# Kernel optimization log

Measured on AMD Instinct MI355X. Metric: run time of the kernel, lower is better.

Reference implementation:

```python
import jax, jax.numpy as jnp
import numpy as np

HID = 1024; INTER = 2048; NSTATE = 16; KCONV = 4; DTRANK = 64
NHEADS = 16; NKV = 4; HDIM = 64; VHDIM = 128; EPS = 1e-6
ATTN_H = HID; K_H = NKV * HDIM; V_H = NKV * VHDIM
LATENT = INTER + ATTN_H + K_H + V_H  # 3840


def rmsnorm(x, w, eps=EPS):
    return x * jax.lax.rsqrt(jnp.mean(x * x, axis=-1, keepdims=True) + eps) * w


def setup_inputs():
    key = jax.random.key(0)
    ks = jax.random.split(key, 8)
    B, S = 2, 2048
    s = 0.02
    x = jax.random.normal(ks[0], (B, S, HID), jnp.float32)
    W_in = jax.random.normal(ks[1], (LATENT + INTER, HID), jnp.float32) * s
    conv_w = jax.random.normal(ks[2], (INTER, KCONV), jnp.float32) * 0.2
    conv_b = jnp.zeros((INTER,), jnp.float32)
    W_x = jax.random.normal(ks[3], (DTRANK + 2 * NSTATE, INTER), jnp.float32) * s
    dt_ln_w = jnp.ones((DTRANK,), jnp.float32)
    B_ln_w = jnp.ones((NSTATE,), jnp.float32)
    C_ln_w = jnp.ones((NSTATE,), jnp.float32)
    W_dt = jax.random.normal(ks[4], (INTER, DTRANK), jnp.float32) * s
    b_dt = jnp.log(jnp.expm1(jnp.full((INTER,), 0.01, jnp.float32)))
    A_log = jnp.log(jnp.broadcast_to(jnp.arange(1, NSTATE + 1, dtype=jnp.float32)[None, :], (INTER, NSTATE)))
    D_param = jnp.ones((INTER,), jnp.float32)
    ln1_w = jnp.ones((INTER,), jnp.float32)
    ln2_w = jnp.ones((INTER,), jnp.float32)
    W_out = jax.random.normal(ks[5], (HID, INTER), jnp.float32) * s
    return {"x": x, "W_in": W_in, "conv_w": conv_w, "conv_b": conv_b, "W_x": W_x,
            "dt_ln_w": dt_ln_w, "B_ln_w": B_ln_w, "C_ln_w": C_ln_w, "W_dt": W_dt,
            "b_dt": b_dt, "A_log": A_log, "D_param": D_param, "ln1_w": ln1_w,
            "ln2_w": ln2_w, "W_out": W_out}


def reference(x, W_in, conv_w, conv_b, W_x, dt_ln_w, B_ln_w, C_ln_w, W_dt, b_dt,
              A_log, D_param, ln1_w, ln2_w, W_out):
    Bsz, S, _ = x.shape
    proj = x @ W_in.T  # [B,S,LATENT+INTER]
    q = proj[..., :ATTN_H]
    k = proj[..., ATTN_H:ATTN_H + K_H]
    v = proj[..., ATTN_H + K_H:ATTN_H + K_H + V_H]
    xs = proj[..., ATTN_H + K_H + V_H:LATENT]
    gate = proj[..., LATENT:]

    # depthwise causal conv1d + silu (causal_conv1d_fn)
    xt = xs.transpose(0, 2, 1)  # [B,D,S]
    xc = jax.lax.conv_general_dilated(xt, conv_w[:, None, :], (1,), [(KCONV - 1, 0)],
                                      feature_group_count=INTER,
                                      dimension_numbers=("NCH", "OIH", "NCH"))
    xc = jax.nn.silu(xc + conv_b[None, :, None]).transpose(0, 2, 1)  # [B,S,D]

    # input-dependent dt, B, C with inner RMSNorms
    ssm_p = xc @ W_x.T  # [B,S,DTRANK+2N]
    dt = rmsnorm(ssm_p[..., :DTRANK], dt_ln_w)
    Bm = rmsnorm(ssm_p[..., DTRANK:DTRANK + NSTATE], B_ln_w)
    Cm = rmsnorm(ssm_p[..., DTRANK + NSTATE:], C_ln_w)
    delta = jax.nn.softplus(dt @ W_dt.T + b_dt)  # [B,S,D] (delta_bias + softplus)
    A = -jnp.exp(A_log)  # [D,N]

    def step(h, inp):
        d_t, b_t, c_t, x_t = inp  # [B,D],[B,N],[B,N],[B,D]
        dA = jnp.exp(d_t[:, :, None] * A)  # [B,D,N]
        h = h * dA + (d_t * x_t)[:, :, None] * b_t[:, None, :]
        y = jnp.einsum("bdn,bn->bd", h, c_t)
        return h, y

    h0 = jnp.zeros((Bsz, INTER, NSTATE), x.dtype)
    _, ys = jax.lax.scan(step, h0, (delta.transpose(1, 0, 2), Bm.transpose(1, 0, 2),
                                    Cm.transpose(1, 0, 2), xc.transpose(1, 0, 2)))
    y = ys.transpose(1, 0, 2) + xc * D_param
    y = y * jax.nn.silu(gate)  # gated scan output [B,S,INTER]

    # causal GQA attention branch (no output proj; v_head_dim = INTER/NHEADS)
    qh = q.reshape(Bsz, S, NHEADS, HDIM).transpose(0, 2, 1, 3)
    kh = jnp.repeat(k.reshape(Bsz, S, NKV, HDIM), NHEADS // NKV, axis=2).transpose(0, 2, 1, 3)
    vh = jnp.repeat(v.reshape(Bsz, S, NKV, VHDIM), NHEADS // NKV, axis=2).transpose(0, 2, 1, 3)
    scores = jnp.einsum("bhqd,bhkd->bhqk", qh, kh) * (1.0 / float(np.sqrt(HDIM)))
    mask = jnp.tril(jnp.ones((S, S), bool))
    scores = jnp.where(mask, scores, jnp.finfo(scores.dtype).min)
    attn = jnp.einsum("bhqk,bhkd->bhqd", jax.nn.softmax(scores, axis=-1), vh)
    attn = attn.transpose(0, 2, 1, 3).reshape(Bsz, S, INTER)

    out = (rmsnorm(attn, ln1_w) + rmsnorm(y, ln2_w)) * 0.5
    return out @ W_out.T
```

## Files before the change

### kernel.cpp

```cpp
#include <hip/hip_runtime.h>
#include <stdint.h>

#define HID    1024
#define INTER  2048
#define NSTATE 16
#define DTRANK 64
#define NHEADS 16
#define NKV    4
#define HDIM   64
#define VHDIM  128
#define ATTN_H 1024
#define K_H    256
#define V_H    512
#define LATENT 3840
#define NCOLS  5888
#define BATCH  2
#define SEQ    2048
#define T_TOT  4096
#define NCHUNK 64
#define CHLEN  32
#define LOG2E  1.44269504f

typedef __bf16 bf16x8 __attribute__((ext_vector_type(8)));
typedef float  f32x4  __attribute__((ext_vector_type(4)));
typedef float  f32x4v __attribute__((ext_vector_type(4)));
typedef unsigned short u16x8 __attribute__((ext_vector_type(8)));

__device__ __forceinline__ float bf2f(unsigned short u) {
    return __uint_as_float(((unsigned int)u) << 16);
}
__device__ __forceinline__ unsigned short f2bf(float f) {
    unsigned int u = __float_as_uint(f);
    u = (u + 0x7fffu + ((u >> 16) & 1u)) >> 16;
    return (unsigned short)u;
}
__device__ __forceinline__ bf16x8 ldb8(const unsigned short* p) {
    return __builtin_bit_cast(bf16x8, *(const u16x8*)p);
}

typedef const __attribute__((address_space(1))) unsigned int* gas_ptr;
typedef __attribute__((address_space(3))) unsigned int* las_ptr;
__device__ __forceinline__ void load_lds16(const void* g, void* l) {
    __builtin_amdgcn_global_load_lds((gas_ptr)g, (las_ptr)l, 16, 0, 0);
}

__global__ void k_prep(const float* __restrict__ x, const float* __restrict__ W_in,
                       const float* __restrict__ W_dt, const float* __restrict__ W_out,
                       const float* __restrict__ W_x,
                       unsigned short* __restrict__ xbf, unsigned short* __restrict__ Winbf,
                       unsigned short* __restrict__ Wdtbf, unsigned short* __restrict__ Woutbf,
                       unsigned short* __restrict__ Wxpad) {
    int i = blockIdx.x * 256 + threadIdx.x;
    const float* src; unsigned short* dst; int off;
    if (i < 524288)        { src = x;     dst = xbf;    off = i; }
    else if (i < 1277952)  { src = W_in;  dst = Winbf;  off = i - 524288; }
    else if (i < 1294336)  { src = W_dt;  dst = Wdtbf;  off = i - 1277952; }
    else if (i < 1556480)  { src = W_out; dst = Woutbf; off = i - 1294336; }
    else {
        int e = (i - 1556480) * 8;
        int row = e >> 11, col = e & 2047;
        u16x8 o;
        if (row < DTRANK + 2 * NSTATE) {
#pragma unroll
            for (int k = 0; k < 8; k++) o[k] = f2bf(W_x[(size_t)row * INTER + col + k]);
        } else {
#pragma unroll
            for (int k = 0; k < 8; k++) o[k] = 0;
        }
        *(u16x8*)(Wxpad + e) = o;
        return;
    }
    f32x4v a = ((const f32x4v*)src)[2 * off];
    f32x4v b = ((const f32x4v*)src)[2 * off + 1];
    u16x8 o;
#pragma unroll
    for (int k = 0; k < 4; k++) { o[k] = f2bf(a[k]); o[k + 4] = f2bf(b[k]); }
    *(u16x8*)(dst + (size_t)off * 8) = o;
}

template <int OUT_MODE>
__launch_bounds__(256)
__global__ void k_gemm(const unsigned short* __restrict__ A, const unsigned short* __restrict__ B,
                       void* __restrict__ Cout, const float* __restrict__ bias,
                       int M, int N, int K, int lda, int ldb, int ldc) {
    __shared__ __align__(16) unsigned short As[128 * 64];
    __shared__ __align__(16) unsigned short Bs[128 * 64];
    const int tid = threadIdx.x;
    const int lane = tid & 63;
    const int w = tid >> 6;
    const int wm = w >> 1, wn = w & 1;
    const int nwg = gridDim.x * gridDim.y;
    int lin = blockIdx.y * gridDim.x + blockIdx.x;
    lin = (lin & 7) * (nwg >> 3) + (lin >> 3);
    const int bm = (lin / gridDim.x) * 128, bn = (lin % gridDim.x) * 128;
    const size_t koff = (OUT_MODE == 3) ? (size_t)blockIdx.z * K : 0;

    f32x4 acc[4][4];
#pragma unroll
    for (int i = 0; i < 4; i++)
#pragma unroll
        for (int j = 0; j < 4; j++) acc[i][j] = (f32x4){0.f, 0.f, 0.f, 0.f};

    const int nk = K >> 6;
    for (int ks = 0; ks < nk; ++ks) {
        const int k0 = ks << 6;
#pragma unroll
        for (int i = 0; i < 4; ++i) {
            int qb = (w << 6) + (i << 8);
            int q = qb + lane;
            int row = q >> 3, c = q & 7;
            int csrc = c ^ (row & 7);
            load_lds16(A + (size_t)(bm + row) * lda + koff + k0 + csrc * 8, As + qb * 8);
            load_lds16(B + (size_t)(bn + row) * ldb + koff + k0 + csrc * 8, Bs + qb * 8);
        }
        __syncthreads();
#pragma unroll
        for (int kk = 0; kk < 2; ++kk) {
            bf16x8 af[4], bfr[4];
#pragma unroll
            for (int mi = 0; mi < 4; mi++) {
                int row = (wm << 6) + (mi << 4) + (lane & 15);
                int c = (kk << 2) + (lane >> 4);
                af[mi] = ldb8(As + row * 64 + (c ^ (row & 7)) * 8);
            }
#pragma unroll
            for (int ni = 0; ni < 4; ni++) {
                int row = (wn << 6) + (ni << 4) + (lane & 15);
                int c = (kk << 2) + (lane >> 4);
                bfr[ni] = ldb8(Bs + row * 64 + (c ^ (row & 7)) * 8);
            }
#pragma unroll
            for (int mi = 0; mi < 4; mi++)
#pragma unroll
                for (int ni = 0; ni < 4; ni++)
                    acc[mi][ni] = __builtin_amdgcn_mfma_f32_16x16x32_bf16(af[mi], bfr[ni], acc[mi][ni], 0, 0, 0);
        }
        __syncthreads();
    }
#pragma unroll
    for (int mi = 0; mi < 4; mi++)
#pragma unroll
        for (int ni = 0; ni < 4; ni++)
#pragma unroll
            for (int r = 0; r < 4; r++) {
                int grow = bm + (wm << 6) + (mi << 4) + ((lane >> 4) << 2) + r;
                int gcol = bn + (wn << 6) + (ni << 4) + (lane & 15);
                float v = acc[mi][ni][r];
                if (OUT_MODE == 0) {
                    ((unsigned short*)Cout)[(size_t)grow * ldc + gcol] = f2bf(v);
                } else if (OUT_MODE == 1) {
                    ((float*)Cout)[(size_t)grow * ldc + gcol] = v;
                } else if (OUT_MODE == 3) {
                    ((float*)Cout)[(size_t)blockIdx.z * M * ldc + (size_t)grow * ldc + gcol] = v;
                } else {
                    v += bias[gcol];
                    v = (v > 20.f) ? v : log1pf(__expf(v));
                    ((unsigned short*)Cout)[(size_t)grow * ldc + gcol] = f2bf(v);
                }
            }
}

__global__ void k_conv(const unsigned short* __restrict__ proj, const float* __restrict__ conv_w,
                       const float* __restrict__ conv_b, unsigned short* __restrict__ xc) {
    int r = blockIdx.x;
    int d8 = threadIdx.x * 8;
    int t = r & (SEQ - 1);
    float accv[8];
#pragma unroll
    for (int i = 0; i < 8; i++) accv[i] = conv_b[d8 + i];
#pragma unroll
    for (int j = 0; j < 4; j++) {
        int tp = t - 3 + j;
        if (tp < 0) continue;
        u16x8 xv = *(const u16x8*)(proj + (size_t)(r - 3 + j) * NCOLS + (LATENT - INTER) + d8);
#pragma unroll
        for (int i = 0; i < 8; i++) accv[i] += conv_w[(d8 + i) * 4 + j] * bf2f(xv[i]);
    }
    u16x8 o;
#pragma unroll
    for (int i = 0; i < 8; i++) {
        float v = accv[i];
        v = v / (1.f + __expf(-v));
        o[i] = f2bf(v);
    }
    *(u16x8*)(xc + (size_t)r * INTER + d8) = o;
}

__global__ void k_rms3(const float* __restrict__ ssmp, const float* __restrict__ dt_w,
                       const float* __restrict__ B_w, const float* __restrict__ C_w,
                       unsigned short* __restrict__ dtbf, float* __restrict__ Bm, float* __restrict__ Cm) {
    int r = blockIdx.x;
    int tid = threadIdx.x;
    int lane = tid & 63, w = tid >> 6;
    int c = tid;
    float v = 0.f;
    if (c < 96) {
#pragma unroll
        for (int s = 0; s < 8; s++) v += ssmp[(size_t)s * (T_TOT * 128) + (size_t)r * 128 + c];
    }
    float s = v * v;
    if (w == 0) {
#pragma unroll
        for (int d = 1; d < 64; d <<= 1) s += __shfl_xor(s, d);
        float rms = rsqrtf(s * (1.f / 64.f) + 1e-6f);
        dtbf[(size_t)r * 64 + lane] = f2bf(v * rms * dt_w[lane]);
    } else {
#pragma unroll
        for (int d = 1; d < 16; d <<= 1) s += __shfl_xor(s, d);
        float rms = rsqrtf(s * (1.f / 16.f) + 1e-6f);
        if (lane < 16) Bm[(size_t)r * 16 + lane] = v * rms * B_w[lane];
        else if (lane < 32) Cm[(size_t)r * 16 + (lane - 16)] = v * rms * C_w[lane - 16];
    }
}

template <int PASS>
__launch_bounds__(256)
__global__ void k_scan_chunk(const unsigned short* __restrict__ deltabf, const unsigned short* __restrict__ xcbf,
                             const float* __restrict__ Bm, const float* __restrict__ Cm,
                             const float* __restrict__ A_log,
                             float* __restrict__ hend, float* __restrict__ sumd,
                             const float* __restrict__ hinit, unsigned short* __restrict__ ybf) {
    __shared__ __align__(16) unsigned short dltS[CHLEN * 256];
    __shared__ __align__(16) unsigned short xvS[CHLEN * 256];
    __shared__ __align__(16) float BsT[CHLEN * 16];
    __shared__ __align__(16) float CsT[CHLEN * 16];
    const int d0 = blockIdx.x * 256;
    const int c = blockIdx.y;
    const int b = blockIdx.z;
    const int tid = threadIdx.x, lane = tid & 63, w = tid >> 6;
    const int t0 = c * CHLEN;
    const size_t rowbase = (size_t)(b * SEQ + t0);

    float An[16];
    {
        const f32x4* ap = (const f32x4*)(A_log + (size_t)(d0 + tid) * 16);
#pragma unroll
        for (int n4 = 0; n4 < 4; n4++) {
            f32x4 av = ap[n4];
#pragma unroll
            for (int j = 0; j < 4; j++) An[n4 * 4 + j] = -LOG2E * __expf(av[j]);
        }
    }

#pragma unroll
    for (int i = 0; i < 4; ++i) {
        int qb = (w << 6) + (i << 8);
        int q = qb + lane;
        int t = q >> 5, coff = q & 31;
        load_lds16(deltabf + (rowbase + t) * INTER + d0 + coff * 8, dltS + qb * 8);
        load_lds16(xcbf + (rowbase + t) * INTER + d0 + coff * 8, xvS + qb * 8);
    }
    if (tid < 128) {
        ((f32x4*)BsT)[tid] = ((const f32x4*)(Bm + rowbase * 16))[tid];
        if (PASS == 2) ((f32x4*)CsT)[tid] = ((const f32x4*)(Cm + rowbase * 16))[tid];
    }
    __syncthreads();

    const size_t sidx = ((size_t)(c * BATCH + b) * INTER + d0 + tid) * 16;
    float h[16];
    if (PASS == 2) {
        const f32x4* hp = (const f32x4*)(hinit + sidx);
#pragma unroll
        for (int n4 = 0; n4 < 4; n4++) {
            f32x4 hv = hp[n4];
#pragma unroll
            for (int j = 0; j < 4; j++) h[n4 * 4 + j] = hv[j];
        }
    } else {
#pragma unroll
        for (int n = 0; n < 16; n++) h[n] = 0.f;
    }
    float sd = 0.f;
    for (int t = 0; t < CHLEN; ++t) {
        float dlt = bf2f(dltS[t * 256 + tid]);
        float xv = bf2f(xvS[t * 256 + tid]);
        float dx = dlt * xv;
        if (PASS == 0) sd += dlt;
        float y = 0.f;
#pragma unroll
        for (int n4 = 0; n4 < 4; ++n4) {
            f32x4 Bt = ((f32x4*)BsT)[t * 4 + n4];
            f32x4 Ct;
            if (PASS == 2) Ct = ((f32x4*)CsT)[t * 4 + n4];
#pragma unroll
            for (int j = 0; j < 4; ++j) {
                int n = n4 * 4 + j;
                float a = exp2f(dlt * An[n]);
                h[n] = h[n] * a + dx * Bt[j];
                if (PASS == 2) y += h[n] * Ct[j];
            }
        }
        if (PASS == 2) ybf[(rowbase + t) * INTER + d0 + tid] = f2bf(y);
    }
    if (PASS == 0) {
        f32x4* hp = (f32x4*)(hend + sidx);
#pragma unroll
        for (int n4 = 0; n4 < 4; n4++) {
            f32x4 hv;
#pragma unroll
            for (int j = 0; j < 4; j++) hv[j] = h[n4 * 4 + j];
            hp[n4] = hv;
        }
        sumd[(size_t)(c * BATCH + b) * INTER + d0 + tid] = sd;
    }
}

__global__ void k_scan_prop(const float* __restrict__ A_log, const float* __restrict__ hend,
                            const float* __restrict__ sumd, float* __restrict__ hinit) {
    const int tid = blockIdx.x * 256 + threadIdx.x;
    const int n = tid & 15;
    const int d = (tid >> 4) & (INTER - 1);
    const float An = -LOG2E * __expf(A_log[(size_t)d * 16 + n]);
    const int bd = tid >> 4;
    float h = 0.f;
#pragma unroll 1
    for (int cb = 0; cb < NCHUNK / 4; ++cb) {
        float he[4], sdv[4];
#pragma unroll
        for (int j = 0; j < 4; j++) {
            int c = cb * 4 + j;
            he[j] = hend[(size_t)c * 65536 + tid];
            sdv[j] = sumd[(size_t)c * 4096 + bd];
        }
#pragma unroll
        for (int j = 0; j < 4; j++) {
            int c = cb * 4 + j;
            hinit[(size_t)c * 65536 + tid] = h;
            h = he[j] + exp2f(An * sdv[j]) * h;
        }
    }
}

__launch_bounds__(256)
__global__ void k_attn(const unsigned short* __restrict__ proj, unsigned short* __restrict__ attn) {
    __shared__ __align__(16) unsigned short Ks[64 * 64];
    __shared__ __align__(16) unsigned short Vt[128 * 64];
    __shared__ __align__(16) unsigned short Ps[4 * 16 * 64];
    const int pair = blockIdx.x;
    const int h = blockIdx.y;
    const int b = blockIdx.z;
    const int g = h >> 2;
    const int tid = threadIdx.x, lane = tid & 63, w = tid >> 6;
    const int l15 = lane & 15, hi = lane >> 4;

    const int krow = tid >> 3, kc = tid & 7;
    const int kp2 = (tid & 31) * 2, vb = tid >> 5;

    const unsigned short* kbase = proj + (size_t)(b * SEQ) * NCOLS + ATTN_H + g * HDIM;
    const unsigned short* vbase = proj + (size_t)(b * SEQ) * NCOLS + (ATTN_H + K_H) + g * VHDIM;

    u16x8 krA[2], vrA[2][2], krB[2], vrB[2][2];

    auto LOAD = [&](u16x8* kr, u16x8 (*vr)[2], int kv) {
        const unsigned short* kp_ = kbase + (size_t)(kv + krow) * NCOLS + kc * 8;
        kr[0] = *(const u16x8*)kp_;
        kr[1] = *(const u16x8*)(kp_ + (size_t)32 * NCOLS);
        const unsigned short* vp_ = vbase + (size_t)(kv + kp2) * NCOLS + vb * 8;
        vr[0][0] = *(const u16x8*)vp_;
        vr[0][1] = *(const u16x8*)(vp_ + NCOLS);
        vr[1][0] = *(const u16x8*)(vp_ + 64);
        vr[1][1] = *(const u16x8*)(vp_ + NCOLS + 64);
    };
    auto WRITE = [&](u16x8* kr, u16x8 (*vr)[2]) {
        int ksw = (kc ^ (krow & 7)) << 3;
        *(u16x8*)&Ks[krow * 64 + ksw] = kr[0];
        *(u16x8*)&Ks[(krow + 32) * 64 + ksw] = kr[1];
#pragma unroll
        for (int hf = 0; hf < 2; hf++) {
            u16x8 va = vr[hf][0], vb2 = vr[hf][1];
#pragma unroll
            for (int i = 0; i < 8; i++) {
                unsigned int pk = (unsigned int)va[i] | ((unsigned int)vb2[i] << 16);
                int r = (vb + hf * 8) * 8 + i;
                *(unsigned int*)&Vt[r * 64 + (((kp2 >> 3) ^ (r & 7)) << 3) + (kp2 & 7)] = pk;
            }
        }
    };

    const float SC = 0.18033688f;

    for (int phase = 0; phase < 2; ++phase) {
        const int qt = (phase == 0) ? (31 - pair) : pair;
        const int qw = qt * 64 + w * 16;
        const int ntiles = qt + 1;

        bf16x8 qf[2];
        {
            int qr = qw + l15;
            const unsigned short* qp = proj + (size_t)(b * SEQ + qr) * NCOLS + h * HDIM + hi * 8;
            qf[0] = ldb8(qp);
            qf[1] = ldb8(qp + 32);
        }
        f32x4 O[8];
#pragma unroll
        for (int vf = 0; vf < 8; vf++) O[vf] = (f32x4){0.f, 0.f, 0.f, 0.f};
        float l_[4] = {0.f, 0.f, 0.f, 0.f};

        auto COMPUTE = [&](int kv, bool MASK) {
            const int pbase = w * 1024;
            f32x4 sv[4];
#pragma unroll
            for (int cf = 0; cf < 4; ++cf) {
                f32x4 s = (f32x4){0.f, 0.f, 0.f, 0.f};
                int row = cf * 16 + l15;
#pragma unroll
                for (int kk = 0; kk < 2; ++kk) {
                    bf16x8 kb = ldb8(&Ks[row * 64 + ((((kk << 2) + hi) ^ (row & 7)) << 3)]);
                    s = __builtin_amdgcn_mfma_f32_16x16x32_bf16(qf[kk], kb, s, 0, 0, 0);
                }
                sv[cf] = s;
            }
            const int qi0 = qw + (hi << 2);
#pragma unroll
            for (int cf = 0; cf < 4; ++cf) {
                int ki = kv + cf * 16 + l15;
#pragma unroll
                for (int rg = 0; rg < 4; ++rg) {
                    float v;
                    if (MASK) v = (ki <= qi0 + rg) ? exp2f(sv[cf][rg] * SC) : 0.f;
                    else      v = exp2f(sv[cf][rg] * SC);
                    l_[rg] += v;
                    int pr = (hi << 2) + rg;
                    int pc = cf * 16 + l15;
                    Ps[pbase + pr * 64 + (((pc >> 3) ^ (pr & 7)) << 3) + (pc & 7)] = f2bf(v);
                }
            }
            bf16x8 pa0 = ldb8(&Ps[pbase + l15 * 64 + ((hi ^ (l15 & 7)) << 3)]);
            bf16x8 pa1 = ldb8(&Ps[pbase + l15 * 64 + (((4 + hi) ^ (l15 & 7)) << 3)]);
#pragma unroll
            for (int vf = 0; vf < 8; ++vf) {
                int vr_ = vf * 16 + l15;
                bf16x8 v0 = ldb8(&Vt[vr_ * 64 + ((hi ^ (vr_ & 7)) << 3)]);
                bf16x8 v1 = ldb8(&Vt[vr_ * 64 + (((4 + hi) ^ (vr_ & 7)) << 3)]);
                O[vf] = __builtin_amdgcn_mfma_f32_16x16x32_bf16(pa0, v0, O[vf], 0, 0, 0);
                O[vf] = __builtin_amdgcn_mfma_f32_16x16x32_bf16(pa1, v1, O[vf], 0, 0, 0);
            }
        };

        LOAD(krA, vrA, 0);
        bool useA = true;
        for (int j = 0; j < ntiles; ++j) {
            if (useA) {
                WRITE(krA, vrA);
                if (j + 1 < ntiles) LOAD(krB, vrB, (j + 1) * 64);
            } else {
                WRITE(krB, vrB);
                if (j + 1 < ntiles) LOAD(krA, vrA, (j + 1) * 64);
            }
            __syncthreads();
            COMPUTE(j * 64, j == ntiles - 1);
            __syncthreads();
            useA = !useA;
        }

#pragma unroll
        for (int dd = 1; dd < 16; dd <<= 1)
#pragma unroll
            for (int rg = 0; rg < 4; ++rg) l_[rg] += __shfl_xor(l_[rg], dd);
#pragma unroll
        for (int rg = 0; rg < 4; ++rg) {
            float inv = 1.f / l_[rg];
            int grow = b * SEQ + qw + (hi << 2) + rg;
#pragma unroll
            for (int vf = 0; vf < 8; ++vf) {
                int gcol = h * VHDIM + vf * 16 + l15;
                attn[(size_t)grow * INTER + gcol] = f2bf(O[vf][rg] * inv);
            }
        }
    }
}

__launch_bounds__(256)
__global__ void k_fuse(const unsigned short* __restrict__ attn, const unsigned short* __restrict__ ybf,
                       const unsigned short* __restrict__ xc, const unsigned short* __restrict__ proj,
                       const float* __restrict__ Dp, const float* __restrict__ ln1,
                       const float* __restrict__ ln2, unsigned short* __restrict__ fused) {
    __shared__ float red[8];
    int r = blockIdx.x, tid = threadIdx.x;
    int c8 = tid * 8;
    u16x8 av = *(const u16x8*)(attn + (size_t)r * INTER + c8);
    u16x8 yv8 = *(const u16x8*)(ybf + (size_t)r * INTER + c8);
    u16x8 xv8 = *(const u16x8*)(xc + (size_t)r * INTER + c8);
    u16x8 gv8 = *(const u16x8*)(proj + (size_t)r * NCOLS + LATENT + c8);
    float a_[8], y_[8];
    float ssa = 0.f, ssy = 0.f;
#pragma unroll
    for (int i = 0; i < 8; i++) {
        float a = bf2f(av[i]);
        float yv = bf2f(yv8[i]) + bf2f(xv8[i]) * Dp[c8 + i];
        float gg = bf2f(gv8[i]);
        yv *= gg / (1.f + __expf(-gg));
        a_[i] = a; y_[i] = yv;
        ssa += a * a; ssy += yv * yv;
    }
#pragma unroll
    for (int d = 1; d < 64; d <<= 1) { ssa += __shfl_xor(ssa, d); ssy += __shfl_xor(ssy, d); }
    int w = tid >> 6, lane = tid & 63;
    if (lane == 0) { red[w * 2] = ssa; red[w * 2 + 1] = ssy; }
    __syncthreads();
    ssa = red[0] + red[2] + red[4] + red[6];
    ssy = red[1] + red[3] + red[5] + red[7];
    float ra = rsqrtf(ssa * (1.f / 2048.f) + 1e-6f);
    float ry = rsqrtf(ssy * (1.f / 2048.f) + 1e-6f);
    u16x8 o;
#pragma unroll
    for (int i = 0; i < 8; i++) {
        float v = (a_[i] * ra * ln1[c8 + i] + y_[i] * ry * ln2[c8 + i]) * 0.5f;
        o[i] = f2bf(v);
    }
    *(u16x8*)(fused + (size_t)r * INTER + c8) = o;
}

extern "C" void kernel_launch(void* const* d_in, const int* in_sizes, int n_in,
                              void* d_out, int out_size, void* d_ws, size_t ws_size,
                              hipStream_t stream) {
    const float* x      = (const float*)d_in[0];
    const float* W_in   = (const float*)d_in[1];
    const float* conv_w = (const float*)d_in[2];
    const float* conv_b = (const float*)d_in[3];
    const float* W_x    = (const float*)d_in[4];
    const float* dt_w   = (const float*)d_in[5];
    const float* B_w    = (const float*)d_in[6];
    const float* C_w    = (const float*)d_in[7];
    const float* W_dt   = (const float*)d_in[8];
    const float* b_dt   = (const float*)d_in[9];
    const float* A_log  = (const float*)d_in[10];
    const float* Dp     = (const float*)d_in[11];
    const float* ln1    = (const float*)d_in[12];
    const float* ln2    = (const float*)d_in[13];
    const float* W_out  = (const float*)d_in[14];
    float* out = (float*)d_out;

    char* p = (char*)d_ws;
    auto alloc = [&](size_t bytes) -> void* {
        void* r = (void*)p;
        p += (bytes + 255) & ~(size_t)255;
        return r;
    };
    unsigned short* xbf     = (unsigned short*)alloc((size_t)T_TOT * HID * 2);
    unsigned short* Winbf   = (unsigned short*)alloc((size_t)NCOLS * HID * 2);
    unsigned short* projbf  = (unsigned short*)alloc((size_t)T_TOT * NCOLS * 2);
    unsigned short* xcbf    = (unsigned short*)alloc((size_t)T_TOT * INTER * 2);
    unsigned short* Wxpad   = (unsigned short*)alloc((size_t)128 * INTER * 2);
    float*          ssmp    = (float*)alloc((size_t)8 * T_TOT * 128 * 4);
    unsigned short* dtbf    = (unsigned short*)alloc((size_t)T_TOT * DTRANK * 2);
    float*          Bm      = (float*)alloc((size_t)T_TOT * 16 * 4);
    float*          Cm      = (float*)alloc((size_t)T_TOT * 16 * 4);
    unsigned short* Wdtbf   = (unsigned short*)alloc((size_t)INTER * DTRANK * 2);
    unsigned short* deltabf = (unsigned short*)alloc((size_t)T_TOT * INTER * 2);
    unsigned short* ybf     = (unsigned short*)alloc((size_t)T_TOT * INTER * 2);
    unsigned short* attnbf  = (unsigned short*)alloc((size_t)T_TOT * INTER * 2);
    unsigned short* fusedbf = (unsigned short*)alloc((size_t)T_TOT * INTER * 2);
    unsigned short* Woutbf  = (unsigned short*)alloc((size_t)HID * INTER * 2);
    float*          hendws  = (float*)alloc((size_t)NCHUNK * BATCH * INTER * 16 * 4);
    float*          hinitws = (float*)alloc((size_t)NCHUNK * BATCH * INTER * 16 * 4);
    float*          sumdws  = (float*)alloc((size_t)NCHUNK * BATCH * INTER * 4);

    k_prep<<<6208, 256, 0, stream>>>(x, W_in, W_dt, W_out, W_x, xbf, Winbf, Wdtbf, Woutbf, Wxpad);

    k_gemm<0><<<dim3(NCOLS / 128, T_TOT / 128), 256, 0, stream>>>(
        xbf, Winbf, projbf, nullptr, T_TOT, NCOLS, HID, HID, HID, NCOLS);
    k_conv<<<T_TOT, 256, 0, stream>>>(projbf, conv_w, conv_b, xcbf);
    k_gemm<3><<<dim3(1, T_TOT / 128, 8), 256, 0, stream>>>(
        xcbf, Wxpad, ssmp, nullptr, T_TOT, 128, 256, INTER, INTER, 128);
    k_rms3<<<T_TOT, 128, 0, stream>>>(ssmp, dt_w, B_w, C_w, dtbf, Bm, Cm);
    k_gemm<2><<<dim3(INTER / 128, T_TOT / 128), 256, 0, stream>>>(
        dtbf, Wdtbf, deltabf, b_dt, T_TOT, INTER, DTRANK, DTRANK, DTRANK, INTER);
    k_scan_chunk<0><<<dim3(INTER / 256, NCHUNK, BATCH), 256, 0, stream>>>(
        deltabf, xcbf, Bm, Cm, A_log, hendws, sumdws, nullptr, nullptr);
    k_scan_prop<<<256, 256, 0, stream>>>(A_log, hendws, sumdws, hinitws);
    k_scan_chunk<2><<<dim3(INTER / 256, NCHUNK, BATCH), 256, 0, stream>>>(
        deltabf, xcbf, Bm, Cm, A_log, nullptr, nullptr, hinitws, ybf);
    k_attn<<<dim3(16, NHEADS, BATCH), 256, 0, stream>>>(projbf, attnbf);
    k_fuse<<<T_TOT, 256, 0, stream>>>(attnbf, ybf, xcbf, projbf, Dp, ln1, ln2, fusedbf);
    k_gemm<1><<<dim3(HID / 128, T_TOT / 128), 256, 0, stream>>>(
        fusedbf, Woutbf, out, nullptr, T_TOT, HID, INTER, INTER, INTER, HID);
}
```

Before: 421.8 us.

## Add 256x128 eight-wave double-buffered GEMM for input projection

```diff
diff --git a/kernel.cpp b/kernel.cpp
--- a/kernel.cpp
+++ b/kernel.cpp
@@ -76,6 +76,111 @@
 #pragma unroll
     for (int k = 0; k < 4; k++) { o[k] = f2bf(a[k]); o[k + 4] = f2bf(b[k]); }
     *(u16x8*)(dst + (size_t)off * 8) = o;
+}
+
+template <int NT>
+__launch_bounds__(512)
+__global__ void k_gemm8(const unsigned short* __restrict__ A, const unsigned short* __restrict__ B,
+                        unsigned short* __restrict__ C, int lda, int ldb, int ldc) {
+    __shared__ __align__(16) unsigned short As[2][256 * 64];
+    __shared__ __align__(16) unsigned short Bs[2][128 * 64];
+    const int tid = threadIdx.x;
+    const int lane = tid & 63;
+    const int w = tid >> 6;
+    const int wm = w >> 2, wn = w & 3;
+    const int l15 = lane & 15, hi = lane >> 4;
+    const int nwg = gridDim.x * gridDim.y;
+    int lin = blockIdx.y * gridDim.x + blockIdx.x;
+    lin = (lin & 7) * (nwg >> 3) + (lin >> 3);
+    const int bm = (lin / gridDim.x) * 256;
+    const int bn = (lin % gridDim.x) * 128;
+
+    const int srcCol = ((lane & 7) ^ (lane >> 3)) * 8;
+
+    auto stageA = [&](int buf, int kt, int mh) {
+#pragma unroll
+        for (int j = 0; j < 2; ++j) {
+            int rsb = 64 * mh + 128 * j + 8 * w;
+            int grow = bm + rsb + (lane >> 3);
+            load_lds16(A + (size_t)grow * lda + kt * 64 + srcCol, &As[buf][rsb * 64]);
+        }
+    };
+    auto stageB = [&](int buf, int kt, int nh) {
+        int rsb = 32 * (w >> 1) + 16 * nh + 8 * (w & 1);
+        int grow = bn + rsb + (lane >> 3);
+        load_lds16(B + (size_t)grow * ldb + kt * 64 + srcCol, &Bs[buf][rsb * 64]);
+    };
+
+    f32x4 acc[8][2];
+#pragma unroll
+    for (int i = 0; i < 8; i++)
+#pragma unroll
+        for (int j = 0; j < 2; j++) acc[i][j] = (f32x4){0.f, 0.f, 0.f, 0.f};
+
+    auto phase = [&](int buf, int mh, int nh, auto stageThunk, int vm) {
+        bf16x8 a_[4][2], b_[2];
+#pragma unroll
+        for (int mi4 = 0; mi4 < 4; ++mi4) {
+            int row = 128 * wm + 64 * mh + 16 * mi4 + l15;
+#pragma unroll
+            for (int kk = 0; kk < 2; ++kk) {
+                int cc = (kk << 2) + hi;
+                a_[mi4][kk] = ldb8(&As[buf][row * 64 + ((cc ^ (row & 7)) << 3)]);
+            }
+        }
+        {
+            int row = 32 * wn + 16 * nh + l15;
+#pragma unroll
+            for (int kk = 0; kk < 2; ++kk) {
+                int cc = (kk << 2) + hi;
+                b_[kk] = ldb8(&Bs[buf][row * 64 + ((cc ^ (row & 7)) << 3)]);
+            }
+        }
+        stageThunk();
+        if (vm == 1)      asm volatile("s_waitcnt vmcnt(3)" ::: "memory");
+        else if (vm == 2) asm volatile("s_waitcnt vmcnt(0)" ::: "memory");
+        __builtin_amdgcn_s_barrier();
+        __builtin_amdgcn_s_setprio(1);
+#pragma unroll
+        for (int kk = 0; kk < 2; ++kk)
+#pragma unroll
+            for (int mi4 = 0; mi4 < 4; ++mi4)
+                acc[4 * mh + mi4][nh] =
+                    __builtin_amdgcn_mfma_f32_16x16x32_bf16(a_[mi4][kk], b_[kk], acc[4 * mh + mi4][nh], 0, 0, 0);
+        __builtin_amdgcn_s_setprio(0);
+        __builtin_amdgcn_s_barrier();
+    };
+
+    stageA(0, 0, 0); stageB(0, 0, 0); stageA(0, 0, 1); stageB(0, 0, 1);
+    stageA(1, 1, 0); stageB(1, 1, 0);
+    asm volatile("s_waitcnt vmcnt(3)" ::: "memory");
+    __builtin_amdgcn_s_barrier();
+
+    const int NIT = NT / 2;
+    for (int i = 0; i < NIT; ++i) {
+        const int t1 = 2 * i + 1, t2 = 2 * i + 2, t3 = 2 * i + 3;
+        const bool s2 = t2 < NT, s3 = t3 < NT;
+        const bool last = (i == NIT - 1);
+        phase(0, 0, 0, [&] { stageA(1, t1, 1); }, 0);
+        phase(0, 0, 1, [&] { stageB(1, t1, 1); }, 0);
+        phase(0, 1, 0, [&] { if (s2) stageA(0, t2, 0); }, 0);
+        phase(0, 1, 1, [&] { if (s2) stageB(0, t2, 0); }, last ? 2 : 1);
+        phase(1, 0, 0, [&] { if (s2) stageA(0, t2, 1); }, 0);
+        phase(1, 0, 1, [&] { if (s2) stageB(0, t2, 1); }, 0);
+        phase(1, 1, 0, [&] { if (s3) stageA(1, t3, 0); }, 0);
+        phase(1, 1, 1, [&] { if (s3) stageB(1, t3, 0); }, last ? 0 : 1);
+    }
+
+#pragma unroll
+    for (int mi = 0; mi < 8; ++mi)
+#pragma unroll
+        for (int ni = 0; ni < 2; ++ni)
+#pragma unroll
+            for (int r = 0; r < 4; ++r) {
+                int grow = bm + 128 * wm + 16 * mi + (hi << 2) + r;
+                int gcol = bn + 32 * wn + 16 * ni + l15;
+                C[(size_t)grow * ldc + gcol] = f2bf(acc[mi][ni][r]);
+            }
 }
 
 template <int OUT_MODE>
@@ -558,8 +663,8 @@
 
     k_prep<<<6208, 256, 0, stream>>>(x, W_in, W_dt, W_out, W_x, xbf, Winbf, Wdtbf, Woutbf, Wxpad);
 
-    k_gemm<0><<<dim3(NCOLS / 128, T_TOT / 128), 256, 0, stream>>>(
-        xbf, Winbf, projbf, nullptr, T_TOT, NCOLS, HID, HID, HID, NCOLS);
+    k_gemm8<16><<<dim3(NCOLS / 128, T_TOT / 256), 512, 0, stream>>>(
+        xbf, Winbf, projbf, HID, HID, NCOLS);
     k_conv<<<T_TOT, 256, 0, stream>>>(projbf, conv_w, conv_b, xcbf);
     k_gemm<3><<<dim3(1, T_TOT / 128, 8), 256, 0, stream>>>(
         xcbf, Wxpad, ssmp, nullptr, T_TOT, 128, 256, INTER, INTER, 128);
```

After: 432.0 us. 2.4% more time.

## Add 256x128 triple-buffered 8-wave GEMM for the input projection

Applied to the files above, without the earlier changes.

```diff
diff --git a/kernel.cpp b/kernel.cpp
--- a/kernel.cpp
+++ b/kernel.cpp
@@ -76,6 +76,102 @@
 #pragma unroll
     for (int k = 0; k < 4; k++) { o[k] = f2bf(a[k]); o[k + 4] = f2bf(b[k]); }
     *(u16x8*)(dst + (size_t)off * 8) = o;
+}
+
+template <int NT>
+__launch_bounds__(512)
+__global__ void k_gemm8(const unsigned short* __restrict__ A, const unsigned short* __restrict__ B,
+                        unsigned short* __restrict__ C, int lda, int ldb, int ldc) {
+    __shared__ __align__(16) unsigned short As[3][256 * 64];
+    __shared__ __align__(16) unsigned short Bs[3][128 * 64];
+    const int tid = threadIdx.x;
+    const int lane = tid & 63;
+    const int w = tid >> 6;
+    const int wm = w >> 1, wn = w & 1;
+    const int l15 = lane & 15, hi = lane >> 4;
+    const int nwg = gridDim.x * gridDim.y;
+    int lin = blockIdx.y * gridDim.x + blockIdx.x;
+    lin = (lin & 7) * (nwg >> 3) + (lin >> 3);
+    const int bm = (lin / gridDim.x) * 256;
+    const int bn = (lin % gridDim.x) * 128;
+
+    const int srcCol = ((lane & 7) ^ (lane >> 3)) * 8;
+
+    auto stageA = [&](int buf, int kt, int u) {
+        int rsb = 64 * u + 8 * w;
+        load_lds16(A + (size_t)(bm + rsb + (lane >> 3)) * lda + kt * 64 + srcCol, &As[buf][rsb * 64]);
+    };
+    auto stageB = [&](int buf, int kt, int u) {
+        int rsb = 64 * u + 8 * w;
+        load_lds16(B + (size_t)(bn + rsb + (lane >> 3)) * ldb + kt * 64 + srcCol, &Bs[buf][rsb * 64]);
+    };
+
+    f32x4 acc[4][4];
+#pragma unroll
+    for (int i = 0; i < 4; i++)
+#pragma unroll
+        for (int j = 0; j < 4; j++) acc[i][j] = (f32x4){0.f, 0.f, 0.f, 0.f};
+
+    auto phase = [&](int buf, int kk, auto stageThunk, int vm) {
+        bf16x8 a_[4], b_[4];
+        const int cc = (kk << 2) + hi;
+#pragma unroll
+        for (int mi = 0; mi < 4; ++mi) {
+            int row = 64 * wm + 16 * mi + l15;
+            a_[mi] = ldb8(&As[buf][row * 64 + ((cc ^ (row & 7)) << 3)]);
+        }
+#pragma unroll
+        for (int ni = 0; ni < 4; ++ni) {
+            int row = 64 * wn + 16 * ni + l15;
+            b_[ni] = ldb8(&Bs[buf][row * 64 + ((cc ^ (row & 7)) << 3)]);
+        }
+        stageThunk();
+        if (vm == 1)      asm volatile("s_waitcnt vmcnt(6)" ::: "memory");
+        else if (vm == 2) asm volatile("s_waitcnt vmcnt(0)" ::: "memory");
+        __builtin_amdgcn_s_barrier();
+        __builtin_amdgcn_s_setprio(1);
+#pragma unroll
+        for (int mi = 0; mi < 4; ++mi)
+#pragma unroll
+            for (int ni = 0; ni < 4; ++ni)
+                acc[mi][ni] = __builtin_amdgcn_mfma_f32_16x16x32_bf16(a_[mi], b_[ni], acc[mi][ni], 0, 0, 0);
+        __builtin_amdgcn_s_setprio(0);
+        __builtin_amdgcn_s_barrier();
+    };
+
+#pragma unroll
+    for (int u = 0; u < 4; ++u) stageA(0, 0, u);
+    stageB(0, 0, 0); stageB(0, 0, 1);
+#pragma unroll
+    for (int u = 0; u < 4; ++u) stageA(1, 1, u);
+    stageB(1, 1, 0); stageB(1, 1, 1);
+    asm volatile("s_waitcnt vmcnt(6)" ::: "memory");
+    __builtin_amdgcn_s_barrier();
+
+    int buf = 0;
+    for (int t = 0; t < NT; ++t) {
+        const int kt = t + 2;
+        const bool st = kt < NT;
+        const int pbuf = (buf + 2 >= 3) ? buf - 1 : buf + 2;
+        phase(buf, 0, [&] {
+            if (st) { stageA(pbuf, kt, 0); stageA(pbuf, kt, 1); stageA(pbuf, kt, 2); }
+        }, 0);
+        phase(buf, 1, [&] {
+            if (st) { stageA(pbuf, kt, 3); stageB(pbuf, kt, 0); stageB(pbuf, kt, 1); }
+        }, st ? 1 : 2);
+        buf = (buf + 1 >= 3) ? 0 : buf + 1;
+    }
+
+#pragma unroll
+    for (int mi = 0; mi < 4; ++mi)
+#pragma unroll
+        for (int ni = 0; ni < 4; ++ni)
+#pragma unroll
+            for (int r = 0; r < 4; ++r) {
+                int grow = bm + 64 * wm + 16 * mi + (hi << 2) + r;
+                int gcol = bn + 64 * wn + 16 * ni + l15;
+                C[(size_t)grow * ldc + gcol] = f2bf(acc[mi][ni][r]);
+            }
 }
 
 template <int OUT_MODE>
@@ -558,8 +654,8 @@
 
     k_prep<<<6208, 256, 0, stream>>>(x, W_in, W_dt, W_out, W_x, xbf, Winbf, Wdtbf, Woutbf, Wxpad);
 
-    k_gemm<0><<<dim3(NCOLS / 128, T_TOT / 128), 256, 0, stream>>>(
-        xbf, Winbf, projbf, nullptr, T_TOT, NCOLS, HID, HID, HID, NCOLS);
+    k_gemm8<16><<<dim3(NCOLS / 128, T_TOT / 256), 512, 0, stream>>>(
+        xbf, Winbf, projbf, HID, HID, NCOLS);
     k_conv<<<T_TOT, 256, 0, stream>>>(projbf, conv_w, conv_b, xcbf);
     k_gemm<3><<<dim3(1, T_TOT / 128, 8), 256, 0, stream>>>(
         xcbf, Wxpad, ssmp, nullptr, T_TOT, 128, 256, INTER, INTER, 128);
```

Measured after the change: 407.8 us. 3.3% less time.
